# Performance work log

Hardware: AMD Instinct MI355X
Metric: run time of the kernel (lower is better)

## Reference

```python
import jax, jax.numpy as jnp
import numpy as np

M_DIM = 32          # vec_dim m
L1 = L2 = L3 = L4 = 3
L_TOT = L1 * L2 * L3 * L4   # 81
R = 2               # rank1..rank4 window size
B_SZ = 4
D_SZ = 16           # D1 = D2 = D3 = D4


def _make_bbasis():
    # Bbasis[idx, i] = prod_k cos(2*pi*(j_k+1)/(i+2)), idx = flattened (j1,j2,j3,j4)
    i = jnp.arange(M_DIM, dtype=jnp.float32)
    def c(Lk):
        j = jnp.arange(Lk, dtype=jnp.float32)
        return jnp.cos(2.0 * jnp.pi * (j[:, None] + 1.0) / (i[None, :] + 2.0))  # [Lk, m]
    c1, c2, c3, c4 = c(L1), c(L2), c(L3), c(L4)
    Bb = (c1[:, None, None, None, :] * c2[None, :, None, None, :]
          * c3[None, None, :, None, :] * c4[None, None, None, :, :])
    return Bb.reshape(L_TOT, M_DIM)


def _window_basis_idx(n1, n2, n3, n4):
    # linear mode, drop: window top-left coords are 0..n_k-1 with step 1
    j1 = jnp.arange(n1) % L1
    j2 = jnp.arange(n2) % L2
    j3 = jnp.arange(n3) % L3
    j4 = jnp.arange(n4) % L4
    idx = (((j1[:, None, None, None] * L2 + j2[None, :, None, None]) * L3
            + j3[None, None, :, None]) * L4 + j4[None, None, None, :])
    return idx.reshape(-1)  # [n_windows]


def setup_inputs() -> dict:
    key = jax.random.key(0)
    k1, k2, k3 = jax.random.split(key, 3)
    arr_batch = jax.random.normal(k1, (B_SZ, D_SZ, D_SZ, D_SZ, D_SZ, M_DIM), dtype=jnp.float32)
    # M initialized near identity (nn.init.eye_ + perturbation so grads are non-trivial)
    M = jnp.eye(M_DIM, dtype=jnp.float32) + 0.01 * jax.random.normal(k2, (M_DIM, M_DIM), dtype=jnp.float32)
    # Acoeff ~ U(-0.1, 0.1) as in reset_parameters
    Acoeff = jax.random.uniform(k3, (M_DIM, L_TOT), dtype=jnp.float32, minval=-0.1, maxval=0.1)
    Bbasis = _make_bbasis()  # fixed buffer, computed deterministically
    return {"arr_batch": arr_batch, "M": M, "Acoeff": Acoeff, "Bbasis": Bbasis}


def reference(arr_batch, M, Acoeff, Bbasis):
    Bsz, D1, D2, D3, D4, m = arr_batch.shape
    # map every vector through M (x @ M.T); avg-pooling commutes with the linear map,
    # matching `mapped = windows @ M.T` then mean over the window
    mapped = jnp.einsum('bpqrsm,nm->bpqrsn', arr_batch, M)
    # 4D sliding window (rank=2 per dim, stride 1, 'drop' -> VALID), rank_op='avg'
    win = (1, R, R, R, R, 1)
    agg = jax.lax.reduce_window(mapped, 0.0, jax.lax.add, win, (1,) * 6, 'VALID') / float(R ** 4)
    n1, n2, n3, n4 = agg.shape[1:5]
    n_win = n1 * n2 * n3 * n4
    agg = agg.reshape(Bsz, n_win, m)            # [B, W, m]
    idx = _window_basis_idx(n1, n2, n3, n4)     # [W]
    phi = Bbasis[idx]                           # [W, m]
    # t_k = Acoeff[:, j_k] * (Bbasis[j_k, :] . agg_k); representation = mean_k t_k
    s = jnp.einsum('bwm,wm->bw', agg, phi)      # [B, W]
    t = s[:, :, None] * Acoeff.T[idx][None]     # [B, W, m]
    return t.mean(axis=1)                       # [B, m]
```

## Files before the change

kernel.cpp:

```cpp
#include <hip/hip_runtime.h>


static __device__ __forceinline__ void add4(float4& a, const float4& b) {
    a.x += b.x; a.y += b.y; a.z += b.z; a.w += b.w;
}
static __device__ __forceinline__ void fma4(float4& a, float w, const float4& b) {
    a.x = fmaf(w, b.x, a.x); a.y = fmaf(w, b.y, a.y);
    a.z = fmaf(w, b.z, a.z); a.w = fmaf(w, b.w, a.w);
}

__global__ __launch_bounds__(128) void sdd4_stage1(
    const float* __restrict__ arr,
    const float* __restrict__ Mmat,
    const float* __restrict__ Bbasis,
    float* __restrict__ S)
{
    __shared__ float4 U_lds[400];
    __shared__ float  V_lds[9 * 33];
    __shared__ float  Y_lds[9 * 33];
    __shared__ float  M_lds[32 * 33];
    __shared__ float  B_lds[81 * 33];

    const int t  = threadIdx.x;
    const int bx = blockIdx.x;
    const int b  = bx >> 8;
    const int p  = (bx >> 4) & 15;
    const int q  = bx & 15;

    const float4* M4 = reinterpret_cast<const float4*>(Mmat);
    for (int i = t; i < 256; i += 128) {
        float4 v = M4[i];
        float* dst = &M_lds[(i >> 3) * 33 + (i & 7) * 4];
        dst[0] = v.x; dst[1] = v.y; dst[2] = v.z; dst[3] = v.w;
    }
    const float4* B4 = reinterpret_cast<const float4*>(Bbasis);
    for (int i = t; i < 648; i += 128) {
        float4 v = B4[i];
        float* dst = &B_lds[(i >> 3) * 33 + (i & 7) * 4];
        dst[0] = v.x; dst[1] = v.y; dst[2] = v.z; dst[3] = v.w;
    }

    const int r  = t >> 3;
    const int mv = t & 7;
    const float4* A4 = reinterpret_cast<const float4*>(arr);
    const size_t tile = (size_t)((b * 16 + p) * 16 + q) * 2048;

    float4 u0 = make_float4(0.f, 0.f, 0.f, 0.f), u1 = u0, u2 = u0;
    #pragma unroll
    for (int s = 0; s < 16; ++s) {
        float4 x = A4[tile + (size_t)(r * 16 + s) * 8 + mv];
        if ((0x36DBu >> s) & 1) add4(u0, x);
        if ((0x6DB6u >> s) & 1) add4(u1, x);
        if ((0xDB6Cu >> s) & 1) add4(u2, x);
    }
    U_lds[r * 25 +      mv] = u0;
    U_lds[r * 25 +  8 + mv] = u1;
    U_lds[r * 25 + 16 + mv] = u2;
    __syncthreads();

    if (t < 72) {
        const int j3  = t / 24;
        const int rem = t % 24;
        const int j4  = rem >> 3;
        const int mv2 = rem & 7;
        const unsigned msk = (j3 == 0) ? 0x36DBu : (j3 == 1 ? 0x6DB6u : 0xDB6Cu);
        float4 acc = make_float4(0.f, 0.f, 0.f, 0.f);
        #pragma unroll
        for (int rr = 0; rr < 16; ++rr) {
            float w = (float)((msk >> rr) & 1u);
            fma4(acc, w, U_lds[rr * 25 + j4 * 8 + mv2]);
        }
        const int jj = j3 * 3 + j4;
        float* dv = &V_lds[jj * 33 + mv2 * 4];
        dv[0] = acc.x; dv[1] = acc.y; dv[2] = acc.z; dv[3] = acc.w;
    }
    __syncthreads();

    for (int o = t; o < 288; o += 128) {
        const int jj = o >> 5;
        const int n  = o & 31;
        float acc = 0.f;
        #pragma unroll
        for (int m = 0; m < 32; ++m)
            acc = fmaf(M_lds[n * 33 + m], V_lds[jj * 33 + m], acc);
        Y_lds[jj * 33 + n] = acc;
    }
    __syncthreads();

    int l1_0, l1_1 = 0, n1;
    if      (p == 0)  { l1_0 = 0; n1 = 1; }
    else if (p == 15) { l1_0 = 2; n1 = 1; }
    else              { l1_0 = (p - 1) % 3; l1_1 = p % 3; n1 = 2; }
    int l2_0, l2_1 = 0, n2;
    if      (q == 0)  { l2_0 = 0; n2 = 1; }
    else if (q == 15) { l2_0 = 2; n2 = 1; }
    else              { l2_0 = (q - 1) % 3; l2_1 = q % 3; n2 = 2; }

    const int ncomb = n1 * n2 * 9;
    if (t < ncomb) {
        const int jj  = t % 9;
        const int c12 = t / 9;
        const int i1idx = (n2 == 2) ? (c12 >> 1) : c12;
        const int i2idx = (n2 == 2) ? (c12 & 1)  : 0;
        const int i1 = i1idx ? l1_1 : l1_0;
        const int i2 = i2idx ? l2_1 : l2_0;
        const int jf = (i1 * 3 + i2) * 9 + jj;
        float acc = 0.f;
        #pragma unroll
        for (int n = 0; n < 32; ++n)
            acc = fmaf(Y_lds[jj * 33 + n], B_lds[jf * 33 + n], acc);
        atomicAdd(&S[b * 81 + jf], acc);
    }
}

__global__ __launch_bounds__(128) void sdd4_stage2(
    const float* __restrict__ S,
    const float* __restrict__ Acoeff,
    float* __restrict__ out)
{
    const int t = threadIdx.x;
    const int b = t >> 5;
    const int n = t & 31;
    float acc = 0.f;
    #pragma unroll
    for (int j = 0; j < 81; ++j)
        acc = fmaf(Acoeff[n * 81 + j], S[b * 81 + j], acc);
    out[b * 32 + n] = acc * (1.0f / 810000.0f);
}

extern "C" void kernel_launch(void* const* d_in, const int* in_sizes, int n_in,
                              void* d_out, int out_size, void* d_ws, size_t ws_size,
                              hipStream_t stream) {
    const float* arr    = (const float*)d_in[0];
    const float* Mmat   = (const float*)d_in[1];
    const float* Acoeff = (const float*)d_in[2];
    const float* Bbasis = (const float*)d_in[3];
    float* S = (float*)d_ws;

    hipMemsetAsync(d_ws, 0, 4 * 81 * sizeof(float), stream);
    sdd4_stage1<<<dim3(1024), dim3(128), 0, stream>>>(arr, Mmat, Bbasis, S);
    sdd4_stage2<<<dim3(1), dim3(128), 0, stream>>>(S, Acoeff, (float*)d_out);
}
```

Baseline: 86.78 us.

## Precompute Bbasis·M product and fold Acoeff projection into main kernel

```diff
diff --git a/kernel.cpp b/kernel.cpp
--- a/kernel.cpp
+++ b/kernel.cpp
@@ -9,17 +9,57 @@
     a.z = fmaf(w, b.z, a.z); a.w = fmaf(w, b.w, a.w);
 }
 
-__global__ __launch_bounds__(128) void sdd4_stage1(
-    const float* __restrict__ arr,
+__global__ __launch_bounds__(128) void sdd4_prep(
     const float* __restrict__ Mmat,
     const float* __restrict__ Bbasis,
-    float* __restrict__ S)
+    float* __restrict__ G,
+    float* __restrict__ out)
+{
+    __shared__ float M_lds[32 * 33];
+    const int t  = threadIdx.x;
+    const int bx = blockIdx.x;
+
+    const float4* M4 = reinterpret_cast<const float4*>(Mmat);
+    for (int i = t; i < 256; i += 128) {
+        float4 v = M4[i];
+        float* dst = &M_lds[(i >> 3) * 33 + (i & 7) * 4];
+        dst[0] = v.x; dst[1] = v.y; dst[2] = v.z; dst[3] = v.w;
+    }
+    if (bx == 0 && t < 128) out[t] = 0.0f;
+    __syncthreads();
+
+    const int base = bx * 648;
+    for (int k = 0; k < 6; ++k) {
+        const int o = base + t + k * 128;
+        if (o < base + 648) {
+            const int jf = o >> 5, m = o & 31;
+            const float4* Br = reinterpret_cast<const float4*>(Bbasis + jf * 32);
+            float acc = 0.f;
+            #pragma unroll
+            for (int nv = 0; nv < 8; ++nv) {
+                float4 bv = Br[nv];
+                acc = fmaf(bv.x, M_lds[(nv * 4 + 0) * 33 + m], acc);
+                acc = fmaf(bv.y, M_lds[(nv * 4 + 1) * 33 + m], acc);
+                acc = fmaf(bv.z, M_lds[(nv * 4 + 2) * 33 + m], acc);
+                acc = fmaf(bv.w, M_lds[(nv * 4 + 3) * 33 + m], acc);
+            }
+            G[o] = acc;
+        }
+    }
+}
+
+__global__ __launch_bounds__(128) void sdd4_main(
+    const float* __restrict__ arr,
+    const float* __restrict__ G,
+    const float* __restrict__ Acoeff,
+    float* __restrict__ out)
 {
     __shared__ float4 U_lds[400];
     __shared__ float  V_lds[9 * 33];
-    __shared__ float  Y_lds[9 * 33];
-    __shared__ float  M_lds[32 * 33];
-    __shared__ float  B_lds[81 * 33];
+    __shared__ float  G_lds[81 * 33];
+    __shared__ float  A_lds[81 * 33];
+    __shared__ float  c_lds[40];
+    __shared__ int    jf_lds[40];
 
     const int t  = threadIdx.x;
     const int bx = blockIdx.x;
@@ -27,17 +67,16 @@
     const int p  = (bx >> 4) & 15;
     const int q  = bx & 15;
 
-    const float4* M4 = reinterpret_cast<const float4*>(Mmat);
-    for (int i = t; i < 256; i += 128) {
-        float4 v = M4[i];
-        float* dst = &M_lds[(i >> 3) * 33 + (i & 7) * 4];
+    const float4* G4 = reinterpret_cast<const float4*>(G);
+    for (int i = t; i < 648; i += 128) {
+        float4 v = G4[i];
+        float* dst = &G_lds[(i >> 3) * 33 + (i & 7) * 4];
         dst[0] = v.x; dst[1] = v.y; dst[2] = v.z; dst[3] = v.w;
     }
-    const float4* B4 = reinterpret_cast<const float4*>(Bbasis);
-    for (int i = t; i < 648; i += 128) {
-        float4 v = B4[i];
-        float* dst = &B_lds[(i >> 3) * 33 + (i & 7) * 4];
-        dst[0] = v.x; dst[1] = v.y; dst[2] = v.z; dst[3] = v.w;
+    if (t < 81) {
+        #pragma unroll
+        for (int n = 0; n < 32; ++n)
+            A_lds[t * 33 + n] = Acoeff[n * 81 + t];
     }
 
     const int r  = t >> 3;
@@ -76,17 +115,6 @@
     }
     __syncthreads();
 
-    for (int o = t; o < 288; o += 128) {
-        const int jj = o >> 5;
-        const int n  = o & 31;
-        float acc = 0.f;
-        #pragma unroll
-        for (int m = 0; m < 32; ++m)
-            acc = fmaf(M_lds[n * 33 + m], V_lds[jj * 33 + m], acc);
-        Y_lds[jj * 33 + n] = acc;
-    }
-    __syncthreads();
-
     int l1_0, l1_1 = 0, n1;
     if      (p == 0)  { l1_0 = 0; n1 = 1; }
     else if (p == 15) { l1_0 = 2; n1 = 1; }
@@ -107,25 +135,19 @@
         const int jf = (i1 * 3 + i2) * 9 + jj;
         float acc = 0.f;
         #pragma unroll
-        for (int n = 0; n < 32; ++n)
-            acc = fmaf(Y_lds[jj * 33 + n], B_lds[jf * 33 + n], acc);
-        atomicAdd(&S[b * 81 + jf], acc);
+        for (int m = 0; m < 32; ++m)
+            acc = fmaf(G_lds[jf * 33 + m], V_lds[jj * 33 + m], acc);
+        c_lds[t]  = acc;
+        jf_lds[t] = jf;
     }
-}
+    __syncthreads();
 
-__global__ __launch_bounds__(128) void sdd4_stage2(
-    const float* __restrict__ S,
-    const float* __restrict__ Acoeff,
-    float* __restrict__ out)
-{
-    const int t = threadIdx.x;
-    const int b = t >> 5;
-    const int n = t & 31;
-    float acc = 0.f;
-    #pragma unroll
-    for (int j = 0; j < 81; ++j)
-        acc = fmaf(Acoeff[n * 81 + j], S[b * 81 + j], acc);
-    out[b * 32 + n] = acc * (1.0f / 810000.0f);
+    if (t < 32) {
+        float acc = 0.f;
+        for (int k = 0; k < ncomb; ++k)
+            acc = fmaf(A_lds[jf_lds[k] * 33 + t], c_lds[k], acc);
+        atomicAdd(&out[b * 32 + t], acc * (1.0f / 810000.0f));
+    }
 }
 
 extern "C" void kernel_launch(void* const* d_in, const int* in_sizes, int n_in,
@@ -135,9 +157,8 @@
     const float* Mmat   = (const float*)d_in[1];
     const float* Acoeff = (const float*)d_in[2];
     const float* Bbasis = (const float*)d_in[3];
-    float* S = (float*)d_ws;
+    float* G = (float*)d_ws;
 
-    hipMemsetAsync(d_ws, 0, 4 * 81 * sizeof(float), stream);
-    sdd4_stage1<<<dim3(1024), dim3(128), 0, stream>>>(arr, Mmat, Bbasis, S);
-    sdd4_stage2<<<dim3(1), dim3(128), 0, stream>>>(S, Acoeff, (float*)d_out);
+    sdd4_prep<<<dim3(4),    dim3(128), 0, stream>>>(Mmat, Bbasis, G, (float*)d_out);
+    sdd4_main<<<dim3(1024), dim3(128), 0, stream>>>(arr, G, Acoeff, (float*)d_out);
 }
```

Result: slower. 90.36 us (+4.1%).
